# Optimization experiments

Measured on AMD Instinct MI355X. Metric: run time of the kernel, lower is better.

## Reference

```python
import jax, jax.numpy as jnp
import numpy as np

K = 3
KK = K * K
EPS = 1e-5


def conv2d(x, w, b, pad):
    y = jax.lax.conv_general_dilated(x, w, (1, 1), [(pad, pad), (pad, pad)],
                                     dimension_numbers=("NCHW", "OIHW", "NCHW"))
    return y + b[None, :, None, None]


def bn(x, g, b, m, v):
    inv = g / jnp.sqrt(v + EPS)
    return x * inv[None, :, None, None] + (b - m * inv)[None, :, None, None]


def deform_sample(x, dy, dx):
    # x: [B,C,H,W]; dy,dx: [B,KK,H,W] -> sampled [B,C,KK,H,W] (bilinear, zeros outside)
    B, C, H, W = x.shape
    k = jnp.arange(K, dtype=x.dtype) - 1.0  # pad=1, dilation=1, stride=1
    ky = jnp.repeat(k, K)  # [KK] row offsets
    kx = jnp.tile(k, K)    # [KK] col offsets
    hh = jnp.arange(H, dtype=x.dtype)
    ww = jnp.arange(W, dtype=x.dtype)
    py = hh[None, :, None] + ky[:, None, None] + dy  # [B,KK,H,W]
    px = ww[None, None, :] + kx[:, None, None] + dx

    def sample_one(img, py, px):
        y0f = jnp.floor(py); x0f = jnp.floor(px)
        wy = py - y0f; wx = px - x0f
        y0 = y0f.astype(jnp.int32); x0 = x0f.astype(jnp.int32)

        def gather(yi, xi, w):
            valid = (yi >= 0) & (yi < H) & (xi >= 0) & (xi < W)
            yc = jnp.clip(yi, 0, H - 1); xc = jnp.clip(xi, 0, W - 1)
            v = img[:, yc, xc]  # [C,KK,H,W]
            return v * (w * valid)[None]

        return (gather(y0, x0, (1 - wy) * (1 - wx)) +
                gather(y0, x0 + 1, (1 - wy) * wx) +
                gather(y0 + 1, x0, wy * (1 - wx)) +
                gather(y0 + 1, x0 + 1, wy * wx))

    return jax.vmap(sample_one)(x, py, px)


def setup_inputs() -> dict:
    key = jax.random.key(0)
    ks = jax.random.split(key, 16)
    B, C, H, W = 8, 256, 64, 64
    d = {
        "feature": jax.random.normal(ks[0], (B, C, H, W), jnp.float32),
        "p1_w": jax.random.normal(ks[1], (C, C, 1, 1), jnp.float32) * 0.05,
        "p1_b": jax.random.normal(ks[2], (C,), jnp.float32) * 0.05,
        "bn1_g": jax.random.normal(ks[3], (C,), jnp.float32) * 0.1 + 1.0,
        "bn1_b": jax.random.normal(ks[4], (C,), jnp.float32) * 0.05,
        "bn1_m": jax.random.normal(ks[5], (C,), jnp.float32) * 0.05,
        "bn1_v": jax.random.uniform(ks[6], (C,), jnp.float32) + 0.5,
        "off_w": jax.random.normal(ks[7], (3 * KK, 2 * C, K, K), jnp.float32) * 0.01,
        "off_b": jax.random.normal(ks[8], (3 * KK,), jnp.float32) * 0.01,
        "dcn_w": jax.random.normal(ks[9], (C, C, K, K), jnp.float32) * 0.05,
        "dcn_b": jax.random.normal(ks[10], (C,), jnp.float32) * 0.05,
        "bn2_g": jax.random.normal(ks[11], (C,), jnp.float32) * 0.1 + 1.0,
        "bn2_b": jax.random.normal(ks[12], (C,), jnp.float32) * 0.05,
        "bn2_m": jax.random.normal(ks[13], (C,), jnp.float32) * 0.05,
        "bn2_v": jax.random.uniform(ks[14], (C,), jnp.float32) + 0.5,
    }
    return d


def reference(feature, p1_w, p1_b, bn1_g, bn1_b, bn1_m, bn1_v,
              off_w, off_b, dcn_w, dcn_b, bn2_g, bn2_b, bn2_m, bn2_v):
    flipped = feature[..., ::-1]                      # flip last (W) axis
    proj = bn(conv2d(feature, p1_w, p1_b, 0), bn1_g, bn1_b, bn1_m, bn1_v)
    # DCNv2: offsets/mask from concat(flipped, proj)
    concat = jnp.concatenate([flipped, proj], axis=1)
    off = conv2d(concat, off_w, off_b, 1)             # [B,27,H,W]
    dy = off[:, :KK]
    dx = off[:, KK:2 * KK]
    mask = jax.nn.sigmoid(off[:, 2 * KK:])            # [B,KK,H,W]
    sampled = deform_sample(flipped, dy, dx)          # [B,C,KK,H,W]
    O = dcn_w.shape[0]
    y = jnp.einsum("bckhw,ock->bohw", sampled * mask[:, None], dcn_w.reshape(O, -1, KK))
    y = y + dcn_b[None, :, None, None]
    y = bn(y, bn2_g, bn2_b, bn2_m, bn2_v)
    return jax.nn.relu(proj + y)
```

## Files before the change

### kernel.cpp

```cpp
#include <hip/hip_runtime.h>
#include <hip/hip_bf16.h>
#include <math.h>

typedef __attribute__((ext_vector_type(8))) short short8;
typedef __attribute__((ext_vector_type(4))) short short4v;
typedef __attribute__((ext_vector_type(4))) float f32x4;

__device__ __forceinline__ float bs2f(short s){
    union { unsigned u; float f; } x; x.u = ((unsigned)(unsigned short)s) << 16; return x.f;
}
__device__ __forceinline__ short f2bs(float f){
    union { float f; unsigned u; } x; x.f = f;
    unsigned r = x.u + 0x7fff + ((x.u >> 16) & 1);
    return (short)(r >> 16);
}
__device__ __forceinline__ float blo(unsigned u){
    union { unsigned u; float f; } x; x.u = u << 16; return x.f;
}
__device__ __forceinline__ float bhi(unsigned u){
    union { unsigned u; float f; } x; x.u = u & 0xffff0000u; return x.f;
}
__device__ __forceinline__ unsigned pack2(float lo, float hi){
    union { float f; unsigned u; } a, b; a.f = lo; b.f = hi;
    unsigned rl = a.u + 0x7fff + ((a.u >> 16) & 1);
    unsigned rh = b.u + 0x7fff + ((b.u >> 16) & 1);
    return (rl >> 16) | (rh & 0xffff0000u);
}
__device__ __forceinline__ void gl2lds16(const void* g, void* l){
    __builtin_amdgcn_global_load_lds(
        (const __attribute__((address_space(1))) void*)g,
        (__attribute__((address_space(3))) void*)l, 16, 0, 0);
}

#define XPB ((size_t)66*66*512)


__global__ void k_prep(const float* __restrict__ p1_w, const float* __restrict__ p1_b,
                       const float* __restrict__ bn1_g, const float* __restrict__ bn1_b,
                       const float* __restrict__ bn1_m, const float* __restrict__ bn1_v,
                       const float* __restrict__ off_w,
                       const float* __restrict__ dcn_w, const float* __restrict__ dcn_b,
                       const float* __restrict__ bn2_g, const float* __restrict__ bn2_b,
                       const float* __restrict__ bn2_m, const float* __restrict__ bn2_v,
                       short* __restrict__ p1_wb, short* __restrict__ Woffb,
                       short* __restrict__ Wbf,
                       float* __restrict__ bias1f, float* __restrict__ inv2f,
                       float* __restrict__ bias2f, unsigned* __restrict__ XpadU)
{
    int blk = blockIdx.x, t = threadIdx.x;
    if (blk == 0) {
        float inv1 = bn1_g[t] / sqrtf(bn1_v[t] + 1e-5f);
        bias1f[t] = p1_b[t] * inv1 + bn1_b[t] - bn1_m[t] * inv1;
        float inv2 = bn2_g[t] / sqrtf(bn2_v[t] + 1e-5f);
        inv2f[t] = inv2;
        bias2f[t] = dcn_b[t] * inv2 + bn2_b[t] - bn2_m[t] * inv2;
    } else if (blk <= 256) {
        int ci = blk - 1;
        float inv1 = bn1_g[t] / sqrtf(bn1_v[t] + 1e-5f);
        p1_wb[t*256 + ci] = f2bs(p1_w[t*256 + ci] * inv1);
    } else if (blk <= 2560) {
        int ck = blk - 257;
        int c = ck / 9, tap = ck % 9;
        Wbf[t*2304 + tap*256 + c] = f2bs(dcn_w[t*2304 + ck]);
    } else if (blk <= 7168) {
        int e = blk - 2561;
        if (t < 32) {
            int tap = e >> 9, ci = e & 511;
            float v = off_w[((t < 27) ? t : 0)*4608 + ci*9 + tap];
            Woffb[t*4608 + e] = (t < 27) ? f2bs(v) : (short)0;
        }
    } else {
        int hb = blk - 7169;
        int b = hb / 260, i = hb % 260;
        int y, x;
        if (i < 66)       { y = 0;  x = i; }
        else if (i < 132) { y = 65; x = i - 66; }
        else { int j = i - 132; y = 1 + (j >> 1); x = (j & 1) * 65; }
        XpadU[((size_t)(b*66 + y)*66 + x)*256 + t] = 0u;
    }
}

__global__ void k_featT(const float* __restrict__ feature, short* __restrict__ Xpad)
{
    __shared__ float tile[64][65];
    int bb = blockIdx.x;
    int cg = bb & 3, h = (bb >> 2) & 63, b = bb >> 8;
    int c0 = cg * 64;
    int t = threadIdx.x;
    int lw = t & 63, li = t >> 6;
    #pragma unroll
    for (int j = 0; j < 16; ++j) {
        int cl = j*4 + li;
        tile[cl][63 - lw] = feature[((b*256 + c0 + cl)*64 + h)*64 + lw];
    }
    __syncthreads();
    #pragma unroll
    for (int j = 0; j < 16; ++j) {
        int wl = j*4 + li;
        Xpad[((size_t)(b*66 + h+1)*66 + (wl+1))*512 + c0 + lw] = f2bs(tile[lw][wl]);
    }
}

__global__ __launch_bounds__(512, 4) void k_projm(
    short* Xpad, const short* __restrict__ p1_wb, const float* __restrict__ bias1f)
{
    __shared__ short Ash[256*32];
    __shared__ short Bsh[64*32];
    int bid = blockIdx.x;
    int b = bid >> 6, h = bid & 63;
    int t = threadIdx.x;
    int lane = t & 63, w = t >> 6;
    int ln = lane & 15, q = lane >> 4;
    int r16 = lane >> 2;
    int sq  = (lane & 3) ^ ((lane >> 3) & 3);
    int rq  = (q ^ ((ln >> 1) & 3)) * 8;
    size_t rowbase = (size_t)(b*66 + h + 1)*66;

    f32x4 acc[2][4] = {};
    for (int kt = 0; kt < 8; ++kt) {
        int kcol = kt*32 + sq*8;
        #pragma unroll
        for (int i = 0; i < 2; ++i) {
            int row = w*32 + i*16 + r16;
            gl2lds16(p1_wb + (size_t)row*256 + kcol, Ash + (w*32 + i*16)*32);
        }
        if (w < 4) {
            int x = w*16 + r16;
            gl2lds16(Xpad + (rowbase + (64 - x))*512 + kcol, Bsh + (w*16)*32);
        }
        __syncthreads();
        short8 af[2], bfr[4];
        #pragma unroll
        for (int i = 0; i < 2; ++i)
            af[i] = *(const short8*)&Ash[(w*32 + i*16 + ln)*32 + rq];
        #pragma unroll
        for (int j = 0; j < 4; ++j)
            bfr[j] = *(const short8*)&Bsh[(j*16 + ln)*32 + rq];
        #pragma unroll
        for (int i = 0; i < 2; ++i)
            #pragma unroll
            for (int j = 0; j < 4; ++j)
                acc[i][j] = __builtin_amdgcn_mfma_f32_16x16x32_bf16(af[i], bfr[j], acc[i][j], 0, 0, 0);
        __syncthreads();
    }
    #pragma unroll
    for (int i = 0; i < 2; ++i) {
        int ob = w*32 + i*16 + q*4;
        #pragma unroll
        for (int j = 0; j < 4; ++j) {
            int x = j*16 + ln;
            size_t xb = (rowbase + x + 1)*512 + 256 + ob;
            short4v st;
            st.x = f2bs(acc[i][j][0] + bias1f[ob]);
            st.y = f2bs(acc[i][j][1] + bias1f[ob+1]);
            st.z = f2bs(acc[i][j][2] + bias1f[ob+2]);
            st.w = f2bs(acc[i][j][3] + bias1f[ob+3]);
            *(short4v*)&Xpad[xb] = st;
        }
    }
}

__global__ __launch_bounds__(512, 4) void k_offm(
    const short* __restrict__ Xpad, const short* __restrict__ Woffb,
    const float* __restrict__ off_b, float* __restrict__ offv)
{
    __shared__ short Ash[4][32*32];
    __shared__ short Bsh[4][64*32];
    int bid = blockIdx.x;
    int b = bid >> 6, h = bid & 63;
    int t = threadIdx.x;
    int lane = t & 63, w = t >> 6;
    int ln = lane & 15, q = lane >> 4;
    int wr = w >> 2, wc = w & 3;
    int r16 = lane >> 2;
    int sq  = (lane & 3) ^ ((lane >> 3) & 3);
    int rq  = (q ^ ((ln >> 1) & 3)) * 8;
    const short* xb = Xpad + (size_t)b*XPB;

    f32x4 acc = {};
    for (int it = 0; it < 36; ++it) {
        int tap = it >> 2, c0 = (it & 3) << 7;
        int dy = tap/3 - 1, dx = tap%3 - 1;
        #pragma unroll
        for (int s = 0; s < 4; ++s) {
            int cc = c0 + s*32 + sq*8;
            if (w < 4) {
                int row = w*16 + r16;
                const short* gB = xb + ((size_t)(h + 1 + dy)*66 + (row + dx + 1))*512 + cc;
                gl2lds16(gB, &Bsh[s][(w*16)*32]);
            } else if (w < 6) {
                int row = (w-4)*16 + r16;
                const short* gA = Woffb + (size_t)row*4608 + tap*512 + cc;
                gl2lds16(gA, &Ash[s][((w-4)*16)*32]);
            }
        }
        __syncthreads();
        #pragma unroll
        for (int s = 0; s < 4; ++s) {
            short8 af  = *(const short8*)&Ash[s][(wr*16 + ln)*32 + rq];
            short8 bfr = *(const short8*)&Bsh[s][(wc*16 + ln)*32 + rq];
            acc = __builtin_amdgcn_mfma_f32_16x16x32_bf16(af, bfr, acc, 0, 0, 0);
        }
        __syncthreads();
    }
    int x = wc*16 + ln;
    #pragma unroll
    for (int r = 0; r < 4; ++r) {
        int oc = wr*16 + q*4 + r;
        if (oc < 27)
            offv[((b*27 + oc)*64 + h)*64 + x] = acc[r] + off_b[oc];
    }
}

__global__ void k_sample(const short* __restrict__ Xpad,
                         const float* __restrict__ offv,
                         uint2* __restrict__ G)
{
    __shared__ int   c_off[144*4];
    __shared__ float c_w[144*4];
    int bb = blockIdx.x;
    int pg = bb & 3, h = (bb >> 2) & 63, b = bb >> 8;
    int p0 = pg * 16;
    int t = threadIdx.x;

    if (t < 144) {
        int p = p0 + t / 9, k = t % 9;
        int base = (b*27)*4096 + h*64 + p;
        float dy = offv[base + k*4096];
        float dx = offv[base + (9+k)*4096];
        float ms = offv[base + (18+k)*4096];
        ms = 1.f / (1.f + expf(-ms));
        float py = (float)h + (float)(k/3 - 1) + dy;
        float px = (float)p + (float)(k%3 - 1) + dx;
        float y0f = floorf(py), x0f = floorf(px);
        float wy = py - y0f, wx = px - x0f;
        int y0 = (int)y0f, x0 = (int)x0f;
        int y1 = y0 + 1, x1 = x0 + 1;
        float vy0 = (y0 >= 0 && y0 < 64) ? 1.f : 0.f;
        float vy1 = (y1 >= 0 && y1 < 64) ? 1.f : 0.f;
        float vx0 = (x0 >= 0 && x0 < 64) ? 1.f : 0.f;
        float vx1 = (x1 >= 0 && x1 < 64) ? 1.f : 0.f;
        int y0c = min(max(y0,0),63), y1c = min(max(y1,0),63);
        int x0c = min(max(x0,0),63), x1c = min(max(x1,0),63);
        c_off[t*4+0] = ((y0c+1)*66 + x0c+1)*128;
        c_off[t*4+1] = ((y0c+1)*66 + x1c+1)*128;
        c_off[t*4+2] = ((y1c+1)*66 + x0c+1)*128;
        c_off[t*4+3] = ((y1c+1)*66 + x1c+1)*128;
        c_w[t*4+0] = ms * (1.f-wy)*(1.f-wx) * vy0*vx0;
        c_w[t*4+1] = ms * (1.f-wy)*wx       * vy0*vx1;
        c_w[t*4+2] = ms * wy*(1.f-wx)       * vy1*vx0;
        c_w[t*4+3] = ms * wy*wx             * vy1*vx1;
    }
    __syncthreads();

    int tc = t & 63, tg = t >> 6;
    const uint2* fT = (const uint2*)Xpad + (size_t)b*(XPB/4);
    size_t rb = ((size_t)b*4096 + h*64 + p0);
    #pragma unroll
    for (int pi = 0; pi < 4; ++pi) {
        int pl = tg*4 + pi;
        size_t grow = (rb + pl)*576;
        #pragma unroll
        for (int k = 0; k < 9; ++k) {
            int e = pl*9 + k;
            const int4   co = *(const int4*)&c_off[e*4];
            const float4 cw = *(const float4*)&c_w[e*4];
            uint2 u0 = fT[co.x + tc];
            uint2 u1 = fT[co.y + tc];
            uint2 u2 = fT[co.z + tc];
            uint2 u3 = fT[co.w + tc];
            float g0 = cw.x*blo(u0.x) + cw.y*blo(u1.x) + cw.z*blo(u2.x) + cw.w*blo(u3.x);
            float g1 = cw.x*bhi(u0.x) + cw.y*bhi(u1.x) + cw.z*bhi(u2.x) + cw.w*bhi(u3.x);
            float g2 = cw.x*blo(u0.y) + cw.y*blo(u1.y) + cw.z*blo(u2.y) + cw.w*blo(u3.y);
            float g3 = cw.x*bhi(u0.y) + cw.y*bhi(u1.y) + cw.z*bhi(u2.y) + cw.w*bhi(u3.y);
            G[grow + k*64 + tc] = make_uint2(pack2(g0, g1), pack2(g2, g3));
        }
    }
}

__global__ __launch_bounds__(512, 4) void k_gemm(
    const short* __restrict__ G,
    const short* __restrict__ Wbf,
    const short* __restrict__ Xpad,
    const float* __restrict__ inv2f, const float* __restrict__ bias2f,
    float* __restrict__ out)
{
    __shared__ short Ash[2][256*32];
    __shared__ short Bsh[2][64*32];
    int bid = blockIdx.x;
    int n0 = bid * 64;
    int b = n0 >> 12, hw0 = n0 & 4095;
    int t = threadIdx.x;
    int lane = t & 63, w = t >> 6;
    int ln = lane & 15, q = lane >> 4;
    int r16 = lane >> 2;
    int sq  = (lane & 3) ^ ((lane >> 3) & 3);
    int rq  = (q ^ ((ln >> 1) & 3)) * 8;

    f32x4 acc[2][4] = {};
    for (int kc2 = 0; kc2 < 36; ++kc2) {
        #pragma unroll
        for (int s = 0; s < 2; ++s) {
            int kcol = (kc2*2 + s)*32 + sq*8;
            #pragma unroll
            for (int i = 0; i < 2; ++i) {
                int row = w*32 + i*16 + r16;
                gl2lds16(Wbf + (size_t)row*2304 + kcol, &Ash[s][(w*32 + i*16)*32]);
            }
            if (w < 4) {
                int row = w*16 + r16;
                gl2lds16(G + (size_t)(n0 + row)*2304 + kcol, &Bsh[s][(w*16)*32]);
            }
        }
        __syncthreads();
        #pragma unroll
        for (int s = 0; s < 2; ++s) {
            short8 af[2], bfr[4];
            #pragma unroll
            for (int i = 0; i < 2; ++i)
                af[i] = *(const short8*)&Ash[s][(w*32 + i*16 + ln)*32 + rq];
            #pragma unroll
            for (int j = 0; j < 4; ++j)
                bfr[j] = *(const short8*)&Bsh[s][(j*16 + ln)*32 + rq];
            #pragma unroll
            for (int i = 0; i < 2; ++i)
                #pragma unroll
                for (int j = 0; j < 4; ++j)
                    acc[i][j] = __builtin_amdgcn_mfma_f32_16x16x32_bf16(af[i], bfr[j], acc[i][j], 0, 0, 0);
        }
        __syncthreads();
    }

    int h = hw0 >> 6;
    #pragma unroll
    for (int i = 0; i < 2; ++i) {
        int ob = w*32 + i*16 + q*4;
        #pragma unroll
        for (int j = 0; j < 4; ++j) {
            int p = j*16 + ln;
            size_t xb = ((size_t)(b*66 + h + 1)*66 + p + 1)*512 + 256 + ob;
            short4v pr = *(const short4v*)&Xpad[xb];
            #pragma unroll
            for (int r = 0; r < 4; ++r) {
                int o = ob + r;
                size_t idx = ((size_t)(b*256 + o))*4096 + hw0 + p;
                float rs = bs2f(((const short*)&pr)[r]);
                float v = rs + acc[i][j][r]*inv2f[o] + bias2f[o];
                out[idx] = v < 0.f ? 0.f : v;
            }
        }
    }
}

extern "C" void kernel_launch(void* const* d_in, const int* in_sizes, int n_in,
                              void* d_out, int out_size, void* d_ws, size_t ws_size,
                              hipStream_t stream)
{
    const float* feature = (const float*)d_in[0];
    const float* p1_w  = (const float*)d_in[1];
    const float* p1_b  = (const float*)d_in[2];
    const float* bn1_g = (const float*)d_in[3];
    const float* bn1_b = (const float*)d_in[4];
    const float* bn1_m = (const float*)d_in[5];
    const float* bn1_v = (const float*)d_in[6];
    const float* off_w = (const float*)d_in[7];
    const float* off_b = (const float*)d_in[8];
    const float* dcn_w = (const float*)d_in[9];
    const float* dcn_b = (const float*)d_in[10];
    const float* bn2_g = (const float*)d_in[11];
    const float* bn2_b = (const float*)d_in[12];
    const float* bn2_m = (const float*)d_in[13];
    const float* bn2_v = (const float*)d_in[14];

    float* ws = (float*)d_ws;
    short* Xpad   = (short*)ws;
    float* offbuf = ws + 8921088;
    short* p1_wb  = (short*)(ws + 9805824);
    short* Woffb  = (short*)(ws + 9838592);
    short* Wbf    = (short*)(ws + 9912320);
    float* bias1f = ws + 10207232;
    float* inv2f  = ws + 10207488;
    float* bias2f = ws + 10207744;
    short* G      = (short*)(ws + 10208000);

    k_prep<<<9249, 256, 0, stream>>>(p1_w, p1_b, bn1_g, bn1_b, bn1_m, bn1_v,
                                     off_w, dcn_w, dcn_b, bn2_g, bn2_b, bn2_m, bn2_v,
                                     p1_wb, Woffb, Wbf, bias1f, inv2f, bias2f,
                                     (unsigned*)Xpad);
    k_featT<<<2048, 256, 0, stream>>>(feature, Xpad);
    k_projm<<<512, 512, 0, stream>>>(Xpad, p1_wb, bias1f);
    k_offm<<<512, 512, 0, stream>>>(Xpad, Woffb, off_b, offbuf);
    k_sample<<<2048, 256, 0, stream>>>(Xpad, offbuf, (uint2*)G);
    k_gemm<<<512, 512, 0, stream>>>(G, Wbf, Xpad, inv2f, bias2f, (float*)d_out);
}
```

Baseline: 268.4 us.

## Fuse deformable bilinear sampling into the DCN GEMM B-tile producer

Removes the separate sampling kernel and its large intermediate G buffer (B*HW*2304 bf16). The GEMM now computes the bilinear-sampled, mask-weighted columns on the fly for each 64-column K chunk and writes them directly into the swizzled B shared tile. The gathers for the next chunk are prefetched into registers. This saves a full write and read of G in exchange for more register pressure, more LDS for the per-block offset and weight tables, and gather latency inside the GEMM loop. Block indexing is remapped so b varies fastest.

```diff
diff --git a/kernel.cpp b/kernel.cpp
--- a/kernel.cpp
+++ b/kernel.cpp
@@ -212,19 +212,28 @@
     }
 }
 
-__global__ void k_sample(const short* __restrict__ Xpad,
-                         const float* __restrict__ offv,
-                         uint2* __restrict__ G)
-{
-    __shared__ int   c_off[144*4];
-    __shared__ float c_w[144*4];
-    int bb = blockIdx.x;
-    int pg = bb & 3, h = (bb >> 2) & 63, b = bb >> 8;
-    int p0 = pg * 16;
+__global__ __launch_bounds__(512, 4) void k_gemm(
+    const short* __restrict__ Xpad,
+    const short* __restrict__ Wbf,
+    const float* __restrict__ offv,
+    const float* __restrict__ inv2f, const float* __restrict__ bias2f,
+    float* __restrict__ out)
+{
+    __shared__ __align__(16) short Ash[2][256*32];
+    __shared__ __align__(16) short Bsh[2][64*32];
+    __shared__ int   c_off[576*4];
+    __shared__ float c_w[576*4];
+    int bid = blockIdx.x;
+    int b = bid & 7, h = bid >> 3;
     int t = threadIdx.x;
-
-    if (t < 144) {
-        int p = p0 + t / 9, k = t % 9;
+    int lane = t & 63, w = t >> 6;
+    int ln = lane & 15, q = lane >> 4;
+    int r16 = lane >> 2;
+    int sq  = (lane & 3) ^ ((lane >> 3) & 3);
+    int rq  = (q ^ ((ln >> 1) & 3)) * 8;
+
+    for (int e = t; e < 576; e += 512) {
+        int p = e / 9, k = e % 9;
         int base = (b*27)*4096 + h*64 + p;
         float dy = offv[base + k*4096];
         float dx = offv[base + (9+k)*4096];
@@ -242,63 +251,40 @@
         float vx1 = (x1 >= 0 && x1 < 64) ? 1.f : 0.f;
         int y0c = min(max(y0,0),63), y1c = min(max(y1,0),63);
         int x0c = min(max(x0,0),63), x1c = min(max(x1,0),63);
-        c_off[t*4+0] = ((y0c+1)*66 + x0c+1)*128;
-        c_off[t*4+1] = ((y0c+1)*66 + x1c+1)*128;
-        c_off[t*4+2] = ((y1c+1)*66 + x0c+1)*128;
-        c_off[t*4+3] = ((y1c+1)*66 + x1c+1)*128;
-        c_w[t*4+0] = ms * (1.f-wy)*(1.f-wx) * vy0*vx0;
-        c_w[t*4+1] = ms * (1.f-wy)*wx       * vy0*vx1;
-        c_w[t*4+2] = ms * wy*(1.f-wx)       * vy1*vx0;
-        c_w[t*4+3] = ms * wy*wx             * vy1*vx1;
+        c_off[e*4+0] = ((y0c+1)*66 + x0c+1)*128;
+        c_off[e*4+1] = ((y0c+1)*66 + x1c+1)*128;
+        c_off[e*4+2] = ((y1c+1)*66 + x0c+1)*128;
+        c_off[e*4+3] = ((y1c+1)*66 + x1c+1)*128;
+        c_w[e*4+0] = ms * (1.f-wy)*(1.f-wx) * vy0*vx0;
+        c_w[e*4+1] = ms * (1.f-wy)*wx       * vy0*vx1;
+        c_w[e*4+2] = ms * wy*(1.f-wx)       * vy1*vx0;
+        c_w[e*4+3] = ms * wy*wx             * vy1*vx1;
     }
     __syncthreads();
 
-    int tc = t & 63, tg = t >> 6;
     const uint2* fT = (const uint2*)Xpad + (size_t)b*(XPB/4);
-    size_t rb = ((size_t)b*4096 + h*64 + p0);
-    #pragma unroll
-    for (int pi = 0; pi < 4; ++pi) {
-        int pl = tg*4 + pi;
-        size_t grow = (rb + pl)*576;
-        #pragma unroll
-        for (int k = 0; k < 9; ++k) {
-            int e = pl*9 + k;
-            const int4   co = *(const int4*)&c_off[e*4];
-            const float4 cw = *(const float4*)&c_w[e*4];
-            uint2 u0 = fT[co.x + tc];
-            uint2 u1 = fT[co.y + tc];
-            uint2 u2 = fT[co.z + tc];
-            uint2 u3 = fT[co.w + tc];
-            float g0 = cw.x*blo(u0.x) + cw.y*blo(u1.x) + cw.z*blo(u2.x) + cw.w*blo(u3.x);
-            float g1 = cw.x*bhi(u0.x) + cw.y*bhi(u1.x) + cw.z*bhi(u2.x) + cw.w*bhi(u3.x);
-            float g2 = cw.x*blo(u0.y) + cw.y*blo(u1.y) + cw.z*blo(u2.y) + cw.w*blo(u3.y);
-            float g3 = cw.x*bhi(u0.y) + cw.y*bhi(u1.y) + cw.z*bhi(u2.y) + cw.w*bhi(u3.y);
-            G[grow + k*64 + tc] = make_uint2(pack2(g0, g1), pack2(g2, g3));
-        }
-    }
-}
-
-__global__ __launch_bounds__(512, 4) void k_gemm(
-    const short* __restrict__ G,
-    const short* __restrict__ Wbf,
-    const short* __restrict__ Xpad,
-    const float* __restrict__ inv2f, const float* __restrict__ bias2f,
-    float* __restrict__ out)
-{
-    __shared__ short Ash[2][256*32];
-    __shared__ short Bsh[2][64*32];
-    int bid = blockIdx.x;
-    int n0 = bid * 64;
-    int b = n0 >> 12, hw0 = n0 & 4095;
-    int t = threadIdx.x;
-    int lane = t & 63, w = t >> 6;
-    int ln = lane & 15, q = lane >> 4;
-    int r16 = lane >> 2;
-    int sq  = (lane & 3) ^ ((lane >> 3) & 3);
-    int rq  = (q ^ ((ln >> 1) & 3)) * 8;
+    int pr = t >> 3;
+    int jo = t & 7;
+    int pe4 = pr*9*4;
+    short* bdst = &Bsh[jo >> 2][pr*32 + (((jo & 3) ^ ((pr >> 1) & 3)) << 3)];
 
     f32x4 acc[2][4] = {};
+    int4 co = *(const int4*)&c_off[pe4];
+    uint4 u0 = *(const uint4*)(fT + co.x + jo*2);
+    uint4 u1 = *(const uint4*)(fT + co.y + jo*2);
+    uint4 u2 = *(const uint4*)(fT + co.z + jo*2);
+    uint4 u3 = *(const uint4*)(fT + co.w + jo*2);
+
+    #pragma unroll 2
     for (int kc2 = 0; kc2 < 36; ++kc2) {
+        int tap = kc2 >> 2;
+        int kn = kc2 < 35 ? kc2 + 1 : 35;
+        int4 cn = *(const int4*)&c_off[pe4 + (kn >> 2)*4];
+        int cin = ((kn & 3) << 4) + jo*2;
+        uint4 v0 = *(const uint4*)(fT + cn.x + cin);
+        uint4 v1 = *(const uint4*)(fT + cn.y + cin);
+        uint4 v2 = *(const uint4*)(fT + cn.z + cin);
+        uint4 v3 = *(const uint4*)(fT + cn.w + cin);
         #pragma unroll
         for (int s = 0; s < 2; ++s) {
             int kcol = (kc2*2 + s)*32 + sq*8;
@@ -307,11 +293,21 @@
                 int row = w*32 + i*16 + r16;
                 gl2lds16(Wbf + (size_t)row*2304 + kcol, &Ash[s][(w*32 + i*16)*32]);
             }
-            if (w < 4) {
-                int row = w*16 + r16;
-                gl2lds16(G + (size_t)(n0 + row)*2304 + kcol, &Bsh[s][(w*16)*32]);
-            }
-        }
+        }
+        const float4 cw = *(const float4*)&c_w[pe4 + tap*4];
+        float g0 = cw.x*blo(u0.x) + cw.y*blo(u1.x) + cw.z*blo(u2.x) + cw.w*blo(u3.x);
+        float g1 = cw.x*bhi(u0.x) + cw.y*bhi(u1.x) + cw.z*bhi(u2.x) + cw.w*bhi(u3.x);
+        float g2 = cw.x*blo(u0.y) + cw.y*blo(u1.y) + cw.z*blo(u2.y) + cw.w*blo(u3.y);
+        float g3 = cw.x*bhi(u0.y) + cw.y*bhi(u1.y) + cw.z*bhi(u2.y) + cw.w*bhi(u3.y);
+        float g4 = cw.x*blo(u0.z) + cw.y*blo(u1.z) + cw.z*blo(u2.z) + cw.w*blo(u3.z);
+        float g5 = cw.x*bhi(u0.z) + cw.y*bhi(u1.z) + cw.z*bhi(u2.z) + cw.w*bhi(u3.z);
+        float g6 = cw.x*blo(u0.w) + cw.y*blo(u1.w) + cw.z*blo(u2.w) + cw.w*blo(u3.w);
+        float g7 = cw.x*bhi(u0.w) + cw.y*bhi(u1.w) + cw.z*bhi(u2.w) + cw.w*bhi(u3.w);
+        uint4 pk;
+        pk.x = pack2(g0, g1); pk.y = pack2(g2, g3);
+        pk.z = pack2(g4, g5); pk.w = pack2(g6, g7);
+        *(uint4*)bdst = pk;
+        u0 = v0; u1 = v1; u2 = v2; u3 = v3;
         __syncthreads();
         #pragma unroll
         for (int s = 0; s < 2; ++s) {
@@ -320,32 +316,31 @@
             for (int i = 0; i < 2; ++i)
                 af[i] = *(const short8*)&Ash[s][(w*32 + i*16 + ln)*32 + rq];
             #pragma unroll
-            for (int j = 0; j < 4; ++j)
-                bfr[j] = *(const short8*)&Bsh[s][(j*16 + ln)*32 + rq];
+            for (int jj = 0; jj < 4; ++jj)
+                bfr[jj] = *(const short8*)&Bsh[s][(jj*16 + ln)*32 + rq];
             #pragma unroll
             for (int i = 0; i < 2; ++i)
                 #pragma unroll
-                for (int j = 0; j < 4; ++j)
-                    acc[i][j] = __builtin_amdgcn_mfma_f32_16x16x32_bf16(af[i], bfr[j], acc[i][j], 0, 0, 0);
-        }
-        __syncthreads();
-    }
-
-    int h = hw0 >> 6;
+                for (int jj = 0; jj < 4; ++jj)
+                    acc[i][jj] = __builtin_amdgcn_mfma_f32_16x16x32_bf16(af[i], bfr[jj], acc[i][jj], 0, 0, 0);
+        }
+        __syncthreads();
+    }
+
     #pragma unroll
     for (int i = 0; i < 2; ++i) {
         int ob = w*32 + i*16 + q*4;
         #pragma unroll
-        for (int j = 0; j < 4; ++j) {
-            int p = j*16 + ln;
+        for (int jj = 0; jj < 4; ++jj) {
+            int p = jj*16 + ln;
             size_t xb = ((size_t)(b*66 + h + 1)*66 + p + 1)*512 + 256 + ob;
-            short4v pr = *(const short4v*)&Xpad[xb];
+            short4v prr = *(const short4v*)&Xpad[xb];
             #pragma unroll
             for (int r = 0; r < 4; ++r) {
                 int o = ob + r;
-                size_t idx = ((size_t)(b*256 + o))*4096 + hw0 + p;
-                float rs = bs2f(((const short*)&pr)[r]);
-                float v = rs + acc[i][j][r]*inv2f[o] + bias2f[o];
+                size_t idx = ((size_t)(b*256 + o))*4096 + h*64 + p;
+                float rs = bs2f(((const short*)&prr)[r]);
+                float v = rs + acc[i][jj][r]*inv2f[o] + bias2f[o];
                 out[idx] = v < 0.f ? 0.f : v;
             }
         }
@@ -381,7 +376,6 @@
     float* bias1f = ws + 10207232;
     float* inv2f  = ws + 10207488;
     float* bias2f = ws + 10207744;
-    short* G      = (short*)(ws + 10208000);
 
     k_prep<<<9249, 256, 0, stream>>>(p1_w, p1_b, bn1_g, bn1_b, bn1_m, bn1_v,
                                      off_w, dcn_w, dcn_b, bn2_g, bn2_b, bn2_m, bn2_v,
@@ -390,6 +384,5 @@
     k_featT<<<2048, 256, 0, stream>>>(feature, Xpad);
     k_projm<<<512, 512, 0, stream>>>(Xpad, p1_wb, bias1f);
     k_offm<<<512, 512, 0, stream>>>(Xpad, Woffb, off_b, offbuf);
-    k_sample<<<2048, 256, 0, stream>>>(Xpad, offbuf, (uint2*)G);
-    k_gemm<<<512, 512, 0, stream>>>(G, Wbf, Xpad, inv2f, bias2f, (float*)d_out);
-}
+    k_gemm<<<512, 512, 0, stream>>>(Xpad, Wbf, offbuf, inv2f, bias2f, (float*)d_out);
+}
```

New measurement: 234.3 us. 12.7% less time.
